# Performance work log

Measured on AMD Instinct MI355X. Metric: run time of the kernel, lower is better.

## Reference

```python
import jax, jax.numpy as jnp
import numpy as np

VOCAB = 100000
D = 128
B = 256
L = 2048  # leaves per tree (power of two -> complete binary tree)


def setup_inputs() -> dict:
    key = jax.random.key(0)
    k1, k2, k3, k4 = jax.random.split(key, 4)
    word_ids = jax.random.randint(k1, (B, L), 0, VOCAB)
    embedding = jax.random.normal(k2, (VOCAB, D), dtype=jnp.float32) * 0.1
    # torch nn.Linear(2*D, D): weight [D, 2*D], bias [D]
    W = jax.random.normal(k3, (D, 2 * D), dtype=jnp.float32) * (1.0 / np.sqrt(2 * D))
    b = jax.random.normal(k4, (D,), dtype=jnp.float32) * 0.01
    return {"word_ids": word_ids, "embedding": embedding, "W": W, "b": b}


def reference(word_ids, embedding, W, b):
    # Leaves: embedding lookup for every leaf of every tree. [B, L, D]
    x = embedding[word_ids]
    # Internal nodes, batched by depth: each level combines adjacent pairs
    # via linear(concat(left, right)). log2(L) levels (static unroll).
    while x.shape[1] > 1:
        left = x[:, 0::2, :]   # [B, n/2, D]
        right = x[:, 1::2, :]  # [B, n/2, D]
        pair = jnp.concatenate([left, right], axis=-1)  # [B, n/2, 2D]
        x = jnp.einsum('bnd,od->bno', pair, W) + b      # [B, n/2, D]
    return x[:, 0, :]  # root result per tree, [B, D]
```

## Files before the change

kernel.cpp:

```cpp
#include <hip/hip_runtime.h>


typedef __bf16 bf16x8 __attribute__((ext_vector_type(8)));
typedef __bf16 bf16x4 __attribute__((ext_vector_type(4)));
typedef float f32x4 __attribute__((ext_vector_type(4)));

#define STRIDE 136

__global__ void pack_w_kernel(const float* __restrict__ W,
                              __bf16* __restrict__ wpack) {
    const int f = blockIdx.x;
    const int tid = threadIdx.x;
    const int wv = tid >> 6, l = tid & 63;
    const int nl = f >> 3, kk = f & 7;
    const int o = ((wv << 1) + nl) * 16 + (l & 15);
    const int d = kk * 32 + ((l >> 4) << 3);
    const float* src = W + o * 256 + d;
    bf16x8 h;
#pragma unroll
    for (int j = 0; j < 8; ++j) h[j] = (__bf16)src[j];
    *(bf16x8*)(wpack + (size_t)(f * 256 + tid) * 8) = h;
}

template <int NOUT>
__device__ __forceinline__ void level_step(
    const __bf16* src0, const __bf16* src1, __bf16* dst,
    const bf16x8* wf, const float* bval, int wv, int q, int lm)
{
    const int ntm = (NOUT + 15) >> 4;
#pragma unroll
    for (int mt = 0; mt < ntm; ++mt) {
        const __bf16* src = mt ? src1 : src0;
        const int me = (NOUT >= 16) ? lm : (lm < NOUT ? lm : 0);
        f32x4 acc[2];
        acc[0] = f32x4{ bval[0], bval[0], bval[0], bval[0] };
        acc[1] = f32x4{ bval[1], bval[1], bval[1], bval[1] };
#pragma unroll
        for (int kh = 0; kh < 2; ++kh) {
            const int row = 2 * me + kh;
            bf16x8 af[4];
#pragma unroll
            for (int j = 0; j < 4; ++j)
                af[j] = *(const bf16x8*)&src[row * STRIDE + j * 32 + q * 8];
#pragma unroll
            for (int nl = 0; nl < 2; ++nl)
#pragma unroll
                for (int j = 0; j < 4; ++j)
                    acc[nl] = __builtin_amdgcn_mfma_f32_16x16x32_bf16(
                        af[j], wf[nl * 8 + kh * 4 + j], acc[nl], 0, 0, 0);
        }
#pragma unroll
        for (int nl = 0; nl < 2; ++nl) {
            const int col = (2 * wv + nl) * 16 + lm;
            const bf16x4 hv = __builtin_convertvector(acc[nl], bf16x4);
#pragma unroll
            for (int r = 0; r < 4; ++r) {
                const int row = mt * 16 + q * 4 + r;
                if (row < NOUT)
                    dst[row * STRIDE + col] = hv[r];
            }
        }
    }
    __syncthreads();
}

__device__ __forceinline__ void level_final(
    const __bf16* src, __bf16* yrow,
    const bf16x8* wf, const float* bval, int wv, int q, int lm)
{
    const int me = (lm < 2) ? lm : 0;
    f32x4 acc[2];
    acc[0] = f32x4{ bval[0], bval[0], bval[0], bval[0] };
    acc[1] = f32x4{ bval[1], bval[1], bval[1], bval[1] };
#pragma unroll
    for (int kh = 0; kh < 2; ++kh) {
        const int row = 2 * me + kh;
        bf16x8 af[4];
#pragma unroll
        for (int j = 0; j < 4; ++j)
            af[j] = *(const bf16x8*)&src[row * STRIDE + j * 32 + q * 8];
#pragma unroll
        for (int nl = 0; nl < 2; ++nl)
#pragma unroll
            for (int j = 0; j < 4; ++j)
                acc[nl] = __builtin_amdgcn_mfma_f32_16x16x32_bf16(
                    af[j], wf[nl * 8 + kh * 4 + j], acc[nl], 0, 0, 0);
    }
#pragma unroll
    for (int nl = 0; nl < 2; ++nl) {
        const int col = (2 * wv + nl) * 16 + lm;
        if (q == 0) {
            yrow[0 * 128 + col] = (__bf16)acc[nl][0];
            yrow[1 * 128 + col] = (__bf16)acc[nl][1];
        }
    }
}

__device__ __forceinline__ void gather_issue(
    const int* wb64, const float* emb, int tid, f32x4 (&s)[8])
{
#pragma unroll
    for (int i = 0; i < 8; ++i) {
        const int id = wb64[(tid >> 5) + 8 * i];
        s[i] = *(const f32x4*)(emb + (size_t)id * 128 + (tid & 31) * 4);
    }
}

__device__ __forceinline__ void gather_write(
    __bf16* dst, int tid, const f32x4 (&s)[8])
{
#pragma unroll
    for (int i = 0; i < 8; ++i) {
        const int row = (tid >> 5) + 8 * i;
        *(bf16x4*)&dst[row * STRIDE + (tid & 31) * 4] =
            __builtin_convertvector(s[i], bf16x4);
    }
}

__global__ __launch_bounds__(256, 3) void tree128_kernel(
    const int* __restrict__ wid, const float* __restrict__ emb,
    const __bf16* __restrict__ wpack, const float* __restrict__ bias,
    __bf16* __restrict__ yout)
{
    __shared__ __align__(16) __bf16 bufA[64 * STRIDE];
    __shared__ __align__(16) __bf16 bufB[64 * STRIDE];
    __shared__ __align__(16) __bf16 bufC[64 * STRIDE];
    const int tid = threadIdx.x;
    const int batch = blockIdx.x >> 3;
    const int pair = blockIdx.x & 7;
    const int wv = tid >> 6, ln = tid & 63, q = ln >> 4, lm = ln & 15;

    bf16x8 wf[16];
    const bf16x8* wp = (const bf16x8*)wpack;
#pragma unroll
    for (int f = 0; f < 16; ++f) wf[f] = wp[f * 256 + tid];
    float bval[2];
    bval[0] = bias[(2 * wv + 0) * 16 + lm];
    bval[1] = bias[(2 * wv + 1) * 16 + lm];

    const int* wb = wid + batch * 2048 + pair * 256;
    f32x4 st[8];

    gather_issue(wb, emb, tid, st);
    gather_write(bufC, tid, st);
    __syncthreads();

#pragma unroll
    for (int g = 0; g < 2; ++g) {
        const int* wg = wb + g * 128;
        gather_issue(wg + 64, emb, tid, st);
        level_step<32>(bufC, bufC + 32 * STRIDE, bufB, wf, bval, wv, q, lm);
        gather_write(bufA, tid, st);
        __syncthreads();
        level_step<32>(bufA, bufA + 32 * STRIDE, bufB + 32 * STRIDE,
                       wf, bval, wv, q, lm);
        if (g == 0)
            gather_issue(wb + 128, emb, tid, st);
        level_step<32>(bufB, bufB + 32 * STRIDE, bufA, wf, bval, wv, q, lm);
        if (g == 0)
            gather_write(bufC, tid, st);
        level_step<16>(bufA, nullptr, bufB, wf, bval, wv, q, lm);
        level_step<8> (bufB, nullptr, bufA, wf, bval, wv, q, lm);
        level_step<4> (bufA, nullptr, bufB, wf, bval, wv, q, lm);
        level_final(bufB, yout + (size_t)(batch * 32 + (pair * 2 + g) * 2) * 128,
                    wf, bval, wv, q, lm);
        __syncthreads();
    }
}

__global__ __launch_bounds__(256) void tree32_kernel(
    const __bf16* __restrict__ yin, const __bf16* __restrict__ wpack,
    const float* __restrict__ bias, float* __restrict__ out)
{
    __shared__ __align__(16) __bf16 buf0[32 * STRIDE];
    __shared__ __align__(16) __bf16 buf1[16 * STRIDE];
    const int tid = threadIdx.x;
    const int batch = blockIdx.x;
    const int wv = tid >> 6, ln = tid & 63, q = ln >> 4, lm = ln & 15;

    bf16x8 wf[16];
    const bf16x8* wp = (const bf16x8*)wpack;
#pragma unroll
    for (int f = 0; f < 16; ++f) wf[f] = wp[f * 256 + tid];
    float bval[2];
    bval[0] = bias[(2 * wv + 0) * 16 + lm];
    bval[1] = bias[(2 * wv + 1) * 16 + lm];

#pragma unroll
    for (int i = 0; i < 2; ++i) {
        const int flat = tid + 256 * i;
        const int row = flat >> 4;
        const int c8 = flat & 15;
        const bf16x8 v =
            *(const bf16x8*)(yin + (size_t)(batch * 32 + row) * 128 + c8 * 8);
        *(bf16x8*)&buf0[row * STRIDE + c8 * 8] = v;
    }
    __syncthreads();

    level_step<16>(buf0, nullptr, buf1, wf, bval, wv, q, lm);
    level_step<8> (buf1, nullptr, buf0, wf, bval, wv, q, lm);
    level_step<4> (buf0, nullptr, buf1, wf, bval, wv, q, lm);
    level_step<2> (buf1, nullptr, buf0, wf, bval, wv, q, lm);

    {
        f32x4 acc[2];
        acc[0] = f32x4{ bval[0], bval[0], bval[0], bval[0] };
        acc[1] = f32x4{ bval[1], bval[1], bval[1], bval[1] };
#pragma unroll
        for (int kh = 0; kh < 2; ++kh) {
            bf16x8 af[4];
#pragma unroll
            for (int j = 0; j < 4; ++j)
                af[j] = *(const bf16x8*)&buf0[kh * STRIDE + j * 32 + q * 8];
#pragma unroll
            for (int nl = 0; nl < 2; ++nl)
#pragma unroll
                for (int j = 0; j < 4; ++j)
                    acc[nl] = __builtin_amdgcn_mfma_f32_16x16x32_bf16(
                        af[j], wf[nl * 8 + kh * 4 + j], acc[nl], 0, 0, 0);
        }
#pragma unroll
        for (int nl = 0; nl < 2; ++nl) {
            const int col = (2 * wv + nl) * 16 + lm;
            if (q == 0) out[(size_t)batch * 128 + col] = acc[nl][0];
        }
    }
}

extern "C" void kernel_launch(void* const* d_in, const int* in_sizes, int n_in,
                              void* d_out, int out_size, void* d_ws, size_t ws_size,
                              hipStream_t stream) {
    const int*   wid = (const int*)d_in[0];
    const float* emb = (const float*)d_in[1];
    const float* W   = (const float*)d_in[2];
    const float* b   = (const float*)d_in[3];
    float* out = (float*)d_out;

    __bf16* wpack = (__bf16*)d_ws;
    __bf16* y     = wpack + 32768;

    pack_w_kernel<<<16, 256, 0, stream>>>(W, wpack);
    tree128_kernel<<<2048, 256, 0, stream>>>(wid, emb, wpack, b, y);
    tree32_kernel<<<256, 256, 0, stream>>>(y, wpack, b, out);
}
```

Baseline: 128.6 us.

## Restructure per-block tree schedule and interleave two M-tiles in 32-row steps

The block's 256-leaf subtree now runs as one straight-line schedule instead of two 128-leaf halves. It combines earlier, skips one level of small reductions and writes four roots per block directly. The 32-output step now loads both M-tile fragments up front and interleaves four independent MFMA accumulator chains. This is meant to hide MFMA latency and cut barriers and tiny low-utilisation levels. In exchange it uses more registers per thread and changes the buffer reuse pattern, which relies on barrier placement for correctness.

```diff
diff --git a/kernel.cpp b/kernel.cpp
--- a/kernel.cpp
+++ b/kernel.cpp
@@ -22,53 +22,56 @@
     *(bf16x8*)(wpack + (size_t)(f * 256 + tid) * 8) = h;
 }
 
-template <int NOUT>
-__device__ __forceinline__ void level_step(
+__device__ __forceinline__ void step32(
     const __bf16* src0, const __bf16* src1, __bf16* dst,
     const bf16x8* wf, const float* bval, int wv, int q, int lm)
 {
-    const int ntm = (NOUT + 15) >> 4;
-#pragma unroll
-    for (int mt = 0; mt < ntm; ++mt) {
-        const __bf16* src = mt ? src1 : src0;
-        const int me = (NOUT >= 16) ? lm : (lm < NOUT ? lm : 0);
-        f32x4 acc[2];
-        acc[0] = f32x4{ bval[0], bval[0], bval[0], bval[0] };
-        acc[1] = f32x4{ bval[1], bval[1], bval[1], bval[1] };
-#pragma unroll
-        for (int kh = 0; kh < 2; ++kh) {
-            const int row = 2 * me + kh;
-            bf16x8 af[4];
-#pragma unroll
-            for (int j = 0; j < 4; ++j)
-                af[j] = *(const bf16x8*)&src[row * STRIDE + j * 32 + q * 8];
-#pragma unroll
-            for (int nl = 0; nl < 2; ++nl)
-#pragma unroll
-                for (int j = 0; j < 4; ++j)
-                    acc[nl] = __builtin_amdgcn_mfma_f32_16x16x32_bf16(
-                        af[j], wf[nl * 8 + kh * 4 + j], acc[nl], 0, 0, 0);
-        }
+    f32x4 acc[2][2];
+#pragma unroll
+    for (int mt = 0; mt < 2; ++mt)
+#pragma unroll
+        for (int nl = 0; nl < 2; ++nl)
+            acc[mt][nl] = f32x4{ bval[nl], bval[nl], bval[nl], bval[nl] };
+#pragma unroll
+    for (int kh = 0; kh < 2; ++kh) {
+        const int row = 2 * lm + kh;
+        bf16x8 a0[4], a1[4];
+#pragma unroll
+        for (int j = 0; j < 4; ++j) {
+            a0[j] = *(const bf16x8*)&src0[row * STRIDE + j * 32 + q * 8];
+            a1[j] = *(const bf16x8*)&src1[row * STRIDE + j * 32 + q * 8];
+        }
+#pragma unroll
+        for (int j = 0; j < 4; ++j) {
+            acc[0][0] = __builtin_amdgcn_mfma_f32_16x16x32_bf16(
+                a0[j], wf[0 * 8 + kh * 4 + j], acc[0][0], 0, 0, 0);
+            acc[1][0] = __builtin_amdgcn_mfma_f32_16x16x32_bf16(
+                a1[j], wf[0 * 8 + kh * 4 + j], acc[1][0], 0, 0, 0);
+            acc[0][1] = __builtin_amdgcn_mfma_f32_16x16x32_bf16(
+                a0[j], wf[1 * 8 + kh * 4 + j], acc[0][1], 0, 0, 0);
+            acc[1][1] = __builtin_amdgcn_mfma_f32_16x16x32_bf16(
+                a1[j], wf[1 * 8 + kh * 4 + j], acc[1][1], 0, 0, 0);
+        }
+    }
+#pragma unroll
+    for (int mt = 0; mt < 2; ++mt)
 #pragma unroll
         for (int nl = 0; nl < 2; ++nl) {
             const int col = (2 * wv + nl) * 16 + lm;
-            const bf16x4 hv = __builtin_convertvector(acc[nl], bf16x4);
-#pragma unroll
-            for (int r = 0; r < 4; ++r) {
-                const int row = mt * 16 + q * 4 + r;
-                if (row < NOUT)
-                    dst[row * STRIDE + col] = hv[r];
-            }
-        }
-    }
-    __syncthreads();
-}
-
-__device__ __forceinline__ void level_final(
-    const __bf16* src, __bf16* yrow,
+            const bf16x4 hv = __builtin_convertvector(acc[mt][nl], bf16x4);
+#pragma unroll
+            for (int r = 0; r < 4; ++r)
+                dst[(mt * 16 + q * 4 + r) * STRIDE + col] = hv[r];
+        }
+    __syncthreads();
+}
+
+template <int NOUT>
+__device__ __forceinline__ void step_small(
+    const __bf16* src, __bf16* dst,
     const bf16x8* wf, const float* bval, int wv, int q, int lm)
 {
-    const int me = (lm < 2) ? lm : 0;
+    const int me = (NOUT >= 16) ? lm : (lm < NOUT ? lm : 0);
     f32x4 acc[2];
     acc[0] = f32x4{ bval[0], bval[0], bval[0], bval[0] };
     acc[1] = f32x4{ bval[1], bval[1], bval[1], bval[1] };
@@ -89,9 +92,46 @@
 #pragma unroll
     for (int nl = 0; nl < 2; ++nl) {
         const int col = (2 * wv + nl) * 16 + lm;
+        const bf16x4 hv = __builtin_convertvector(acc[nl], bf16x4);
+#pragma unroll
+        for (int r = 0; r < 4; ++r) {
+            const int row = q * 4 + r;
+            if (row < NOUT)
+                dst[row * STRIDE + col] = hv[r];
+        }
+    }
+    __syncthreads();
+}
+
+__device__ __forceinline__ void final4(
+    const __bf16* src, __bf16* yrow,
+    const bf16x8* wf, const float* bval, int wv, int q, int lm)
+{
+    const int me = (lm < 4) ? lm : 0;
+    f32x4 acc[2];
+    acc[0] = f32x4{ bval[0], bval[0], bval[0], bval[0] };
+    acc[1] = f32x4{ bval[1], bval[1], bval[1], bval[1] };
+#pragma unroll
+    for (int kh = 0; kh < 2; ++kh) {
+        const int row = 2 * me + kh;
+        bf16x8 af[4];
+#pragma unroll
+        for (int j = 0; j < 4; ++j)
+            af[j] = *(const bf16x8*)&src[row * STRIDE + j * 32 + q * 8];
+#pragma unroll
+        for (int nl = 0; nl < 2; ++nl)
+#pragma unroll
+            for (int j = 0; j < 4; ++j)
+                acc[nl] = __builtin_amdgcn_mfma_f32_16x16x32_bf16(
+                    af[j], wf[nl * 8 + kh * 4 + j], acc[nl], 0, 0, 0);
+    }
+#pragma unroll
+    for (int nl = 0; nl < 2; ++nl) {
+        const int col = (2 * wv + nl) * 16 + lm;
         if (q == 0) {
-            yrow[0 * 128 + col] = (__bf16)acc[nl][0];
-            yrow[1 * 128 + col] = (__bf16)acc[nl][1];
+#pragma unroll
+            for (int r = 0; r < 4; ++r)
+                yrow[r * 128 + col] = (__bf16)acc[nl][r];
         }
     }
 }
@@ -124,7 +164,7 @@
 {
     __shared__ __align__(16) __bf16 bufA[64 * STRIDE];
     __shared__ __align__(16) __bf16 bufB[64 * STRIDE];
-    __shared__ __align__(16) __bf16 bufC[64 * STRIDE];
+    __shared__ __align__(16) __bf16 bufD[64 * STRIDE];
     const int tid = threadIdx.x;
     const int batch = blockIdx.x >> 3;
     const int pair = blockIdx.x & 7;
@@ -142,30 +182,27 @@
     f32x4 st[8];
 
     gather_issue(wb, emb, tid, st);
-    gather_write(bufC, tid, st);
-    __syncthreads();
-
-#pragma unroll
-    for (int g = 0; g < 2; ++g) {
-        const int* wg = wb + g * 128;
-        gather_issue(wg + 64, emb, tid, st);
-        level_step<32>(bufC, bufC + 32 * STRIDE, bufB, wf, bval, wv, q, lm);
-        gather_write(bufA, tid, st);
-        __syncthreads();
-        level_step<32>(bufA, bufA + 32 * STRIDE, bufB + 32 * STRIDE,
-                       wf, bval, wv, q, lm);
-        if (g == 0)
-            gather_issue(wb + 128, emb, tid, st);
-        level_step<32>(bufB, bufB + 32 * STRIDE, bufA, wf, bval, wv, q, lm);
-        if (g == 0)
-            gather_write(bufC, tid, st);
-        level_step<16>(bufA, nullptr, bufB, wf, bval, wv, q, lm);
-        level_step<8> (bufB, nullptr, bufA, wf, bval, wv, q, lm);
-        level_step<4> (bufA, nullptr, bufB, wf, bval, wv, q, lm);
-        level_final(bufB, yout + (size_t)(batch * 32 + (pair * 2 + g) * 2) * 128,
-                    wf, bval, wv, q, lm);
-        __syncthreads();
-    }
+    gather_write(bufA, tid, st);
+    __syncthreads();
+    gather_issue(wb + 64, emb, tid, st);
+    step32(bufA, bufA + 32 * STRIDE, bufB, wf, bval, wv, q, lm);
+    gather_write(bufA, tid, st);
+    __syncthreads();
+    gather_issue(wb + 128, emb, tid, st);
+    step32(bufA, bufA + 32 * STRIDE, bufB + 32 * STRIDE, wf, bval, wv, q, lm);
+    gather_write(bufA, tid, st);
+    step32(bufB, bufB + 32 * STRIDE, bufD, wf, bval, wv, q, lm);
+    gather_issue(wb + 192, emb, tid, st);
+    step32(bufA, bufA + 32 * STRIDE, bufB, wf, bval, wv, q, lm);
+    gather_write(bufA, tid, st);
+    __syncthreads();
+    step32(bufA, bufA + 32 * STRIDE, bufB + 32 * STRIDE, wf, bval, wv, q, lm);
+    step32(bufB, bufB + 32 * STRIDE, bufD + 32 * STRIDE, wf, bval, wv, q, lm);
+    step32(bufD, bufD + 32 * STRIDE, bufB, wf, bval, wv, q, lm);
+    step_small<16>(bufB, bufD, wf, bval, wv, q, lm);
+    step_small<8>(bufD, bufB, wf, bval, wv, q, lm);
+    final4(bufB, yout + (size_t)(batch * 32 + pair * 4) * 128,
+           wf, bval, wv, q, lm);
 }
 
 __global__ __launch_bounds__(256) void tree32_kernel(
@@ -197,10 +234,10 @@
     }
     __syncthreads();
 
-    level_step<16>(buf0, nullptr, buf1, wf, bval, wv, q, lm);
-    level_step<8> (buf1, nullptr, buf0, wf, bval, wv, q, lm);
-    level_step<4> (buf0, nullptr, buf1, wf, bval, wv, q, lm);
-    level_step<2> (buf1, nullptr, buf0, wf, bval, wv, q, lm);
+    step_small<16>(buf0, buf1, wf, bval, wv, q, lm);
+    step_small<8> (buf1, buf0, wf, bval, wv, q, lm);
+    step_small<4> (buf0, buf1, wf, bval, wv, q, lm);
+    step_small<2> (buf1, buf0, wf, bval, wv, q, lm);
 
     {
         f32x4 acc[2];
```

New measurement: 130.1 us. About the same (+1.2%).
